# Kernel tuning notes

Measured on AMD Instinct MI355X. Metric: run time of the kernel, lower is better.

The kernel has to match this reference:

```python
import jax, jax.numpy as jnp
import numpy as np

N = 2048      # feature_num (nodes/sensors)
T = 5         # timd_num (window length)
D = 64        # embed_dim
TOPK = 21     # topk + 1 (includes self, cos(i,i)=1)
B = 32        # batch
EPS = 1e-5
NEG_SLOPE = 0.2


def setup_inputs() -> dict:
    key = jax.random.key(0)
    ks = jax.random.split(key, 9)
    s = 1.0 / np.sqrt(D)
    return {
        "x": jax.random.normal(ks[0], (B, N, T), jnp.float32),
        "emb": jax.random.normal(ks[1], (N, D), jnp.float32) * s,      # embedding table
        "W": jax.random.normal(ks[2], (D, T), jnp.float32) * (1.0 / np.sqrt(T)),  # GNN lin weight
        "Wb": jax.random.normal(ks[3], (D,), jnp.float32) * 0.01,       # GNN lin bias
        "a_src": jax.random.normal(ks[4], (2 * D,), jnp.float32) * s,   # attention vec (source half)
        "a_dst": jax.random.normal(ks[5], (2 * D,), jnp.float32) * s,   # attention vec (dest half)
        "gamma": jnp.ones((D,), jnp.float32),                            # BatchNorm1d weight
        "beta": jnp.zeros((D,), jnp.float32),                            # BatchNorm1d bias
        "fc_w": jax.random.normal(ks[6], (1, D), jnp.float32) * s,      # fc weight
        "fc_b": jnp.zeros((1,), jnp.float32),                            # fc bias
    }


def reference(x, emb, W, Wb, a_src, a_dst, gamma, beta, fc_w, fc_b):
    # --- cosine-sim topk graph build ---
    norm = jnp.linalg.norm(emb, axis=-1)                    # [N]
    cos = (emb @ emb.T) / (norm[:, None] * norm[None, :])   # [N,N]
    _, idx = jax.lax.top_k(cos, TOPK)                       # [N,TOPK]
    # scatter one-hot adjacency (vectorized, no per-row loop)
    adj = jnp.zeros((N, N), x.dtype).at[jnp.arange(N)[:, None], idx].set(1.0)
    # --- GNN: GDN-style attention message passing ---
    h = jnp.einsum('bnt,dt->bnd', x, W) + Wb                # [B,N,D]
    g = jnp.concatenate([h, jnp.broadcast_to(emb, h.shape)], axis=-1)  # [B,N,2D]
    e_src = g @ a_src                                       # [B,N]
    e_dst = g @ a_dst                                       # [B,N]
    e = jax.nn.leaky_relu(e_src[:, :, None] + e_dst[:, None, :], NEG_SLOPE)  # [B,N,N]
    e = jnp.where(adj > 0, e, jnp.float32(-1e9))
    alpha = jax.nn.softmax(e, axis=-1)                      # [B,N,N], rows sum to 1 over TOPK nbrs
    z = jax.nn.relu(jnp.einsum('bij,bjd->bid', alpha, h))   # [B,N,D]
    # --- output head: z * emb, BN over channels, relu, fc ---
    out = z * emb                                           # [B,N,D]
    mean = out.mean(axis=(0, 1))                            # BN1d stats over (batch, nodes)
    var = out.var(axis=(0, 1))
    out = (out - mean) * jax.lax.rsqrt(var + EPS) * gamma + beta
    out = jax.nn.relu(out)
    out = out @ fc_w.T + fc_b                               # [B,N,1]
    return out.reshape(-1, N)                               # [B,N]
```

## Files before the change

### kernel.cpp

```cpp
#include <hip/hip_runtime.h>
#include <math.h>

#define N_NODES 2048
#define T_WIN 5
#define D_EMB 64
#define TOPK 21
#define B_BATCH 32
#define BN_TOTAL (B_BATCH * N_NODES)
#define EPS_BN 1e-5f
#define NEG_SLOPE 0.2f
#define STATS_STRIDE 16

typedef unsigned long long u64;

__device__ __forceinline__ float wave_sum(float v) {
#pragma unroll
    for (int off = 32; off > 0; off >>= 1) v += __shfl_xor(v, off, 64);
    return v;
}

__device__ __forceinline__ u64 max64(u64 a, u64 b) { return a > b ? a : b; }
__device__ __forceinline__ u64 min64(u64 a, u64 b) { return a < b ? a : b; }

__device__ __forceinline__ u64 bitonic_sort64_desc(u64 key, int lane) {
#pragma unroll
    for (int k = 2; k <= 64; k <<= 1) {
#pragma unroll
        for (int j = k >> 1; j >= 1; j >>= 1) {
            u64 pk = __shfl_xor(key, j, 64);
            bool dirDesc = ((lane & k) == 0);
            bool keepMax = (((lane & j) == 0) == dirDesc);
            key = keepMax ? max64(key, pk) : min64(key, pk);
        }
    }
    return key;
}

__device__ __forceinline__ u64 bitonic_merge_top64(u64 a, u64 b, int lane) {
    u64 br = __shfl(b, 63 - lane, 64);
    u64 c = max64(a, br);
#pragma unroll
    for (int j = 32; j >= 1; j >>= 1) {
        u64 pk = __shfl_xor(c, j, 64);
        bool keepMax = ((lane & j) == 0);
        c = keepMax ? max64(c, pk) : min64(c, pk);
    }
    return c;
}

__global__ __launch_bounds__(256) void k_edge(
    const float* __restrict__ x, const float* __restrict__ W,
    const float* __restrict__ Wb, const float* __restrict__ a_src,
    const float* __restrict__ a_dst, const float* __restrict__ emb,
    float* __restrict__ es2T, float* __restrict__ ed2T,
    float* __restrict__ norms, float* __restrict__ stats,
    float* __restrict__ stats2) {
    if (blockIdx.x < 2) {
        float* p = blockIdx.x ? stats2 : stats;
        ((float4*)p)[threadIdx.x] = make_float4(0.f, 0.f, 0.f, 0.f);
    }
    int wid = threadIdx.x >> 6, lane = threadIdx.x & 63;
    int gw = blockIdx.x * 4 + wid;
    const float* wp = W + lane * T_WIN;
    float w0 = wp[0], w1 = wp[1], w2 = wp[2], w3 = wp[3], w4 = wp[4];
    float bias = Wb[lane];
    float as = a_src[lane], asE = a_src[D_EMB + lane];
    float ad = a_dst[lane], adE = a_dst[D_EMB + lane];

    for (int node = gw; node < BN_TOTAL; node += 8192) {
        int n = node & (N_NODES - 1);
        const float* xp = x + (size_t)node * T_WIN;
        float hv = bias + xp[0] * w0 + xp[1] * w1 + xp[2] * w2 + xp[3] * w3 + xp[4] * w4;
        float e = emb[n * D_EMB + lane];
        if (node < N_NODES) {
            float s2 = wave_sum(e * e);
            if (lane == 0) norms[node] = sqrtf(s2);
        }
        float es = wave_sum(hv * as + e * asE);
        float ed = wave_sum(hv * ad + e * adE);
        if (lane == 0) {
            es2T[node] = es;
            ed2T[node] = ed;
        }
    }
}

__global__ __launch_bounds__(256) void k_gram(
    const float* __restrict__ emb, const float* __restrict__ norms,
    float* __restrict__ cosM) {
    __shared__ __align__(16) float As[64][68];
    __shared__ __align__(16) float Bs[64][68];
    int t = threadIdx.x;
    int g = blockIdx.x;
    int a = (int)((sqrtf(8.f * g + 1.f) - 1.f) * 0.5f);
    while ((a + 1) * (a + 2) / 2 <= g) a++;
    while (a * (a + 1) / 2 > g) a--;
    int bq = g - a * (a + 1) / 2;
    int i0 = a * 64, j0 = bq * 64;

    {
        int r = t >> 2, c0 = t & 3;
        const float4* srcA = (const float4*)(emb + (size_t)(i0 + r) * D_EMB);
        const float4* srcB = (const float4*)(emb + (size_t)(j0 + r) * D_EMB);
#pragma unroll
        for (int k = 0; k < 4; k++) {
            int f4 = c0 + 4 * k;
            float4 v = srcA[f4];
            int d = 4 * f4;
            As[d][r] = v.x; As[d + 1][r] = v.y; As[d + 2][r] = v.z; As[d + 3][r] = v.w;
            float4 w = srcB[f4];
            Bs[d][r] = w.x; Bs[d + 1][r] = w.y; Bs[d + 2][r] = w.z; Bs[d + 3][r] = w.w;
        }
    }
    __syncthreads();

    int ti = t & 15, tj = t >> 4;
    float acc[4][4] = {};
#pragma unroll
    for (int d = 0; d < 64; d++) {
        float4 av = *(const float4*)&As[d][4 * ti];
        float4 bv = *(const float4*)&Bs[d][4 * tj];
        acc[0][0] += av.x * bv.x; acc[0][1] += av.x * bv.y; acc[0][2] += av.x * bv.z; acc[0][3] += av.x * bv.w;
        acc[1][0] += av.y * bv.x; acc[1][1] += av.y * bv.y; acc[1][2] += av.y * bv.z; acc[1][3] += av.y * bv.w;
        acc[2][0] += av.z * bv.x; acc[2][1] += av.z * bv.y; acc[2][2] += av.z * bv.z; acc[2][3] += av.z * bv.w;
        acc[3][0] += av.w * bv.x; acc[3][1] += av.w * bv.y; acc[3][2] += av.w * bv.z; acc[3][3] += av.w * bv.w;
    }

    float nis[4] = {norms[i0 + 4 * ti], norms[i0 + 4 * ti + 1],
                    norms[i0 + 4 * ti + 2], norms[i0 + 4 * ti + 3]};
    float njs[4] = {norms[j0 + 4 * tj], norms[j0 + 4 * tj + 1],
                    norms[j0 + 4 * tj + 2], norms[j0 + 4 * tj + 3]};
#pragma unroll
    for (int r = 0; r < 4; r++) {
        float4 o;
        o.x = acc[r][0] / (nis[r] * njs[0]);
        o.y = acc[r][1] / (nis[r] * njs[1]);
        o.z = acc[r][2] / (nis[r] * njs[2]);
        o.w = acc[r][3] / (nis[r] * njs[3]);
        int i = i0 + 4 * ti + r;
        *(float4*)(cosM + (size_t)i * N_NODES + j0 + 4 * tj) = o;
        cosM[(size_t)(j0 + 4 * tj + 0) * N_NODES + i] = o.x;
        cosM[(size_t)(j0 + 4 * tj + 1) * N_NODES + i] = o.y;
        cosM[(size_t)(j0 + 4 * tj + 2) * N_NODES + i] = o.z;
        cosM[(size_t)(j0 + 4 * tj + 3) * N_NODES + i] = o.w;
    }
}

__global__ __launch_bounds__(256) void k_select(
    const float* __restrict__ cosM, int* __restrict__ idxT) {
    __shared__ u64 candbuf[4][128];
    __shared__ u64 mbuf[2][64];
    int tid = threadIdx.x;
    int wid = tid >> 6, lane = tid & 63;
    int pair = wid >> 1;
    int half = wid & 1;
    int i = blockIdx.x * 2 + pair;
    int jbase = half * (N_NODES / 2);
    const float* row = cosM + (size_t)i * N_NODES + jbase;
    u64* buf = candbuf[wid];

    u64 a = 0;
    u64 t = 0;
    int cnt = 0;
    float vcur = row[lane];

#pragma unroll 1
    for (int c = 0; c < N_NODES / 128; c++) {
        int j = c * 64 + lane;
        float v = vcur;
        if (c < N_NODES / 128 - 1) vcur = row[j + 64];
        unsigned u = __float_as_uint(v);
        u = (u & 0x80000000u) ? ~u : (u | 0x80000000u);
        u64 key = ((u64)u << 32) | (unsigned)(~(j + jbase));
        unsigned long long ball = __ballot(key > t);
        if (ball) {
            int ofs = __popcll(ball & ((1ull << lane) - 1ull));
            if (key > t) buf[cnt + ofs] = key;
            cnt += (int)__popcll(ball);
            if (cnt >= 64) {
                u64 nk = buf[lane];
                nk = bitonic_sort64_desc(nk, lane);
                a = bitonic_merge_top64(a, nk, lane);
                t = __shfl(a, 20, 64);
                int rem = cnt - 64;
                u64 mv = (lane < rem) ? buf[64 + lane] : 0;
                if (lane < rem) buf[lane] = mv;
                cnt = rem;
            }
        }
    }
    while (cnt > 0) {
        int take = cnt < 64 ? cnt : 64;
        u64 nk = (lane < take) ? buf[lane] : 0;
        nk = bitonic_sort64_desc(nk, lane);
        a = bitonic_merge_top64(a, nk, lane);
        t = __shfl(a, 20, 64);
        int rem = cnt - take;
        u64 mv = (lane < rem) ? buf[take + lane] : 0;
        if (lane < rem) buf[lane] = mv;
        cnt = rem;
    }

    if (half) mbuf[pair][lane] = a;
    __syncthreads();
    if (!half) {
        u64 bv = mbuf[pair][lane];
        a = bitonic_merge_top64(a, bv, lane);
        if (lane < TOPK) idxT[lane * N_NODES + i] = (int)(~(unsigned)a);
    }
}

__global__ __launch_bounds__(256) void k_alpha(
    const int* __restrict__ idxT, const float* __restrict__ es2T,
    const float* __restrict__ ed2T, float* __restrict__ alphaT) {
    __shared__ float sed[N_NODES];
    int g = blockIdx.x;
    int b = g & 31;
    int i0 = (g >> 5) * 256;
    int t = threadIdx.x;

    {
        const float4* src = (const float4*)(ed2T + (size_t)b * N_NODES);
        float4* dst = (float4*)sed;
#pragma unroll
        for (int q = 0; q < 2; q++) dst[t + 256 * q] = src[t + 256 * q];
    }
    __syncthreads();

    int i = i0 + t;
    float es = es2T[(size_t)b * N_NODES + i];
    float ev[TOPK];
    float m = -3e38f;
#pragma unroll
    for (int k = 0; k < TOPK; k++) {
        int jk = idxT[k * N_NODES + i];
        float e = es + sed[jk];
        e = e > 0.f ? e : NEG_SLOPE * e;
        ev[k] = e;
        m = fmaxf(m, e);
    }
    float s = 0.f;
#pragma unroll
    for (int k = 0; k < TOPK; k++) {
        ev[k] = __expf(ev[k] - m);
        s += ev[k];
    }
    float inv = 1.0f / s;
#pragma unroll
    for (int k = 0; k < TOPK; k++)
        alphaT[((size_t)b * TOPK + k) * N_NODES + i] = ev[k] * inv;
}

__global__ __launch_bounds__(256, 2) void k_msg(
    const float* __restrict__ x, const float* __restrict__ W,
    const float* __restrict__ Wb, const int* __restrict__ idxT,
    const float* __restrict__ alphaT, const float* __restrict__ emb,
    float* __restrict__ obufT, float* __restrict__ stats,
    float* __restrict__ stats2) {
    __shared__ float hts[N_NODES][6];
    __shared__ float sred[2][4][4];

    int g = blockIdx.x;
    int b = (g & 7) + 8 * ((g >> 3) & 3);
    int c = g >> 5;
    int d0 = c * 4;
    int t = threadIdx.x;
    int wid = t >> 6, lane = t & 63;

    float wc[4][T_WIN], wb4[4];
#pragma unroll
    for (int q = 0; q < 4; q++) {
        wb4[q] = Wb[d0 + q];
#pragma unroll
        for (int tt = 0; tt < T_WIN; tt++) wc[q][tt] = W[(d0 + q) * T_WIN + tt];
    }
    const float* xb = x + (size_t)b * N_NODES * T_WIN;
#pragma unroll
    for (int r = 0; r < 8; r++) {
        int row = t + 256 * r;
        const float* xr = xb + row * T_WIN;
        float x0 = xr[0], x1 = xr[1], x2 = xr[2], x3 = xr[3], x4 = xr[4];
        float h0 = wb4[0] + x0 * wc[0][0] + x1 * wc[0][1] + x2 * wc[0][2] + x3 * wc[0][3] + x4 * wc[0][4];
        float h1 = wb4[1] + x0 * wc[1][0] + x1 * wc[1][1] + x2 * wc[1][2] + x3 * wc[1][3] + x4 * wc[1][4];
        float h2 = wb4[2] + x0 * wc[2][0] + x1 * wc[2][1] + x2 * wc[2][2] + x3 * wc[2][3] + x4 * wc[2][4];
        float h3 = wb4[3] + x0 * wc[3][0] + x1 * wc[3][1] + x2 * wc[3][2] + x3 * wc[3][3] + x4 * wc[3][4];
        *(float2*)&hts[row][0] = make_float2(h0, h1);
        *(float2*)&hts[row][2] = make_float2(h2, h3);
    }
    __syncthreads();

    float sacc[4] = {0.f, 0.f, 0.f, 0.f};
    float sacc2[4] = {0.f, 0.f, 0.f, 0.f};
    const float* aT = alphaT + (size_t)b * TOPK * N_NODES;
#pragma unroll 1
    for (int r = 0; r < 8; r++) {
        int i = 256 * r + t;
        float4 z = make_float4(0.f, 0.f, 0.f, 0.f);
#pragma unroll
        for (int k = 0; k < TOPK; k++) {
            int jk = idxT[k * N_NODES + i];
            float a = aT[(size_t)k * N_NODES + i];
            float2 h01 = *(const float2*)&hts[jk][0];
            float2 h23 = *(const float2*)&hts[jk][2];
            z.x = fmaf(a, h01.x, z.x);
            z.y = fmaf(a, h01.y, z.y);
            z.z = fmaf(a, h23.x, z.z);
            z.w = fmaf(a, h23.y, z.w);
        }
        float4 e4 = *(const float4*)(emb + (size_t)i * D_EMB + d0);
        float4 o;
        o.x = fmaxf(z.x, 0.f) * e4.x;
        o.y = fmaxf(z.y, 0.f) * e4.y;
        o.z = fmaxf(z.z, 0.f) * e4.z;
        o.w = fmaxf(z.w, 0.f) * e4.w;
        ((float4*)obufT)[((size_t)c * B_BATCH + b) * N_NODES + i] = o;
        sacc[0] += o.x; sacc[1] += o.y; sacc[2] += o.z; sacc[3] += o.w;
        sacc2[0] += o.x * o.x; sacc2[1] += o.y * o.y;
        sacc2[2] += o.z * o.z; sacc2[3] += o.w * o.w;
    }

#pragma unroll
    for (int q = 0; q < 4; q++) {
        sacc[q] = wave_sum(sacc[q]);
        sacc2[q] = wave_sum(sacc2[q]);
    }
    if (lane == 0) {
#pragma unroll
        for (int q = 0; q < 4; q++) {
            sred[0][wid][q] = sacc[q];
            sred[1][wid][q] = sacc2[q];
        }
    }
    __syncthreads();
    if (t < 8) {
        int q = t & 3, which = t >> 2;
        float v = sred[which][0][q] + sred[which][1][q] + sred[which][2][q] + sred[which][3][q];
        float* dst = which ? stats2 : stats;
        atomicAdd(&dst[(d0 + q) * STATS_STRIDE], v);
    }
}

__global__ __launch_bounds__(256) void k_out(
    const float* __restrict__ obufT, const float* __restrict__ stats,
    const float* __restrict__ stats2, const float* __restrict__ gamma,
    const float* __restrict__ beta, const float* __restrict__ fc_w,
    const float* __restrict__ fc_b, float* __restrict__ out) {
    __shared__ float smean[64], sinv[64], sg[64], sb[64], sf[64];
    int t = threadIdx.x;
    int g = blockIdx.x;
    int b = g & 31, nc = g >> 5;
    int n = nc * 256 + t;
    const float invM = 1.0f / (float)BN_TOTAL;

    if (t < 64) {
        float mn = stats[t * STATS_STRIDE] * invM;
        float var = stats2[t * STATS_STRIDE] * invM - mn * mn;
        smean[t] = mn;
        sinv[t] = rsqrtf(var + EPS_BN);
        sg[t] = gamma[t]; sb[t] = beta[t]; sf[t] = fc_w[t];
    }
    __syncthreads();

    float fb = fc_b[0];
    float p = 0.f;
#pragma unroll
    for (int c = 0; c < 16; c++) {
        float4 o = ((const float4*)obufT)[((size_t)c * B_BATCH + b) * N_NODES + n];
        int d = 4 * c;
        float v;
        v = fmaxf((o.x - smean[d + 0]) * sinv[d + 0] * sg[d + 0] + sb[d + 0], 0.f); p = fmaf(v, sf[d + 0], p);
        v = fmaxf((o.y - smean[d + 1]) * sinv[d + 1] * sg[d + 1] + sb[d + 1], 0.f); p = fmaf(v, sf[d + 1], p);
        v = fmaxf((o.z - smean[d + 2]) * sinv[d + 2] * sg[d + 2] + sb[d + 2], 0.f); p = fmaf(v, sf[d + 2], p);
        v = fmaxf((o.w - smean[d + 3]) * sinv[d + 3] * sg[d + 3] + sb[d + 3], 0.f); p = fmaf(v, sf[d + 3], p);
    }
    out[b * N_NODES + n] = p + fb;
}

extern "C" void kernel_launch(void* const* d_in, const int* in_sizes, int n_in,
                              void* d_out, int out_size, void* d_ws, size_t ws_size,
                              hipStream_t stream) {
    const float* x     = (const float*)d_in[0];
    const float* emb   = (const float*)d_in[1];
    const float* W     = (const float*)d_in[2];
    const float* Wb    = (const float*)d_in[3];
    const float* a_src = (const float*)d_in[4];
    const float* a_dst = (const float*)d_in[5];
    const float* gamma = (const float*)d_in[6];
    const float* beta  = (const float*)d_in[7];
    const float* fc_w  = (const float*)d_in[8];
    const float* fc_b  = (const float*)d_in[9];
    float* out = (float*)d_out;

    char* ws = (char*)d_ws;
    float* stats  = (float*)(ws + 0);
    float* stats2 = (float*)(ws + 4096);
    int*   idxT   = (int*)  (ws + 8192);
    float* norms  = (float*)(ws + 180224);
    float* es2T   = (float*)(ws + 188416);
    float* ed2T   = (float*)(ws + 450560);
    float* alphaT = (float*)(ws + 712704);
    float* cosM   = (float*)(ws + 6217728);
    float* obufT  = cosM;

    k_edge<<<2048, 256, 0, stream>>>(x, W, Wb, a_src, a_dst, emb,
                                     es2T, ed2T, norms, stats, stats2);
    k_gram<<<528, 256, 0, stream>>>(emb, norms, cosM);
    k_select<<<N_NODES / 2, 256, 0, stream>>>(cosM, idxT);
    k_alpha<<<256, 256, 0, stream>>>(idxT, es2T, ed2T, alphaT);
    k_msg<<<512, 256, 0, stream>>>(x, W, Wb, idxT, alphaT, emb, obufT, stats, stats2);
    k_out<<<256, 256, 0, stream>>>(obufT, stats, stats2, gamma, beta, fc_w, fc_b, out);
}
```

Before: 145.6 us.

## Fold attention vectors into W to precompute per-timestep edge score weights

```diff
diff --git a/kernel.cpp b/kernel.cpp
--- a/kernel.cpp
+++ b/kernel.cpp
@@ -48,40 +48,61 @@
     return c;
 }
 
-__global__ __launch_bounds__(256) void k_edge(
+__global__ __launch_bounds__(256) void k_pre(
     const float* __restrict__ x, const float* __restrict__ W,
     const float* __restrict__ Wb, const float* __restrict__ a_src,
     const float* __restrict__ a_dst, const float* __restrict__ emb,
-    float* __restrict__ es2T, float* __restrict__ ed2T,
+    float* __restrict__ xs2T, float* __restrict__ xd2T,
+    float* __restrict__ es_embP, float* __restrict__ ed_embP,
     float* __restrict__ norms, float* __restrict__ stats,
     float* __restrict__ stats2) {
-    if (blockIdx.x < 2) {
-        float* p = blockIdx.x ? stats2 : stats;
-        ((float4*)p)[threadIdx.x] = make_float4(0.f, 0.f, 0.f, 0.f);
-    }
-    int wid = threadIdx.x >> 6, lane = threadIdx.x & 63;
-    int gw = blockIdx.x * 4 + wid;
-    const float* wp = W + lane * T_WIN;
-    float w0 = wp[0], w1 = wp[1], w2 = wp[2], w3 = wp[3], w4 = wp[4];
-    float bias = Wb[lane];
-    float as = a_src[lane], asE = a_src[D_EMB + lane];
-    float ad = a_dst[lane], adE = a_dst[D_EMB + lane];
-
-    for (int node = gw; node < BN_TOTAL; node += 8192) {
-        int n = node & (N_NODES - 1);
-        const float* xp = x + (size_t)node * T_WIN;
-        float hv = bias + xp[0] * w0 + xp[1] * w1 + xp[2] * w2 + xp[3] * w3 + xp[4] * w4;
-        float e = emb[n * D_EMB + lane];
-        if (node < N_NODES) {
-            float s2 = wave_sum(e * e);
-            if (lane == 0) norms[node] = sqrtf(s2);
-        }
-        float es = wave_sum(hv * as + e * asE);
-        float ed = wave_sum(hv * ad + e * adE);
+    int t = threadIdx.x;
+    if (blockIdx.x < 512) {
+        if (blockIdx.x < 2) {
+            float* p = blockIdx.x ? stats2 : stats;
+            ((float4*)p)[t] = make_float4(0.f, 0.f, 0.f, 0.f);
+        }
+        int wid = t >> 6, lane = t & 63;
+        int node = blockIdx.x * 4 + wid;
+        float e = emb[node * D_EMB + lane];
+        float s2 = wave_sum(e * e);
+        float esE = wave_sum(e * a_src[D_EMB + lane]);
+        float edE = wave_sum(e * a_dst[D_EMB + lane]);
         if (lane == 0) {
-            es2T[node] = es;
-            ed2T[node] = ed;
-        }
+            norms[node] = sqrtf(s2);
+            es_embP[node] = esE;
+            ed_embP[node] = edE;
+        }
+        return;
+    }
+
+    __shared__ float cws[5], cwd[5], cbs[2];
+    if (t < 12) {
+        int which = (t < 5 || t == 10) ? 0 : 1;
+        const float* av = which ? a_dst : a_src;
+        const float* sp;
+        int stride;
+        if (t < 10) { int tt = (t < 5) ? t : t - 5; sp = W + tt; stride = T_WIN; }
+        else        { sp = Wb; stride = 1; }
+        float acc = 0.f;
+        for (int d = 0; d < D_EMB; d++) acc += sp[d * stride] * av[d];
+        if (t < 5)       cws[t] = acc;
+        else if (t < 10) cwd[t - 5] = acc;
+        else             cbs[t - 10] = acc;
+    }
+    __syncthreads();
+    float ws0 = cws[0], ws1 = cws[1], ws2 = cws[2], ws3 = cws[3], ws4 = cws[4];
+    float wd0 = cwd[0], wd1 = cwd[1], wd2 = cwd[2], wd3 = cwd[3], wd4 = cwd[4];
+    float bss = cbs[0], bsd = cbs[1];
+
+    int base = (blockIdx.x - 512) * 1024;
+#pragma unroll
+    for (int r = 0; r < 4; r++) {
+        int item = base + 256 * r + t;
+        const float* xp = x + (size_t)item * T_WIN;
+        float x0 = xp[0], x1 = xp[1], x2 = xp[2], x3 = xp[3], x4 = xp[4];
+        xs2T[item] = bss + x0 * ws0 + x1 * ws1 + x2 * ws2 + x3 * ws3 + x4 * ws4;
+        xd2T[item] = bsd + x0 * wd0 + x1 * wd1 + x2 * wd2 + x3 * wd3 + x4 * wd4;
     }
 }
 
@@ -211,8 +232,9 @@
 }
 
 __global__ __launch_bounds__(256) void k_alpha(
-    const int* __restrict__ idxT, const float* __restrict__ es2T,
-    const float* __restrict__ ed2T, float* __restrict__ alphaT) {
+    const int* __restrict__ idxT, const float* __restrict__ xs2T,
+    const float* __restrict__ xd2T, const float* __restrict__ es_embP,
+    const float* __restrict__ ed_embP, float* __restrict__ alphaT) {
     __shared__ float sed[N_NODES];
     int g = blockIdx.x;
     int b = g & 31;
@@ -220,15 +242,21 @@
     int t = threadIdx.x;
 
     {
-        const float4* src = (const float4*)(ed2T + (size_t)b * N_NODES);
+        const float4* sxd = (const float4*)(xd2T + (size_t)b * N_NODES);
+        const float4* sde = (const float4*)(ed_embP);
         float4* dst = (float4*)sed;
 #pragma unroll
-        for (int q = 0; q < 2; q++) dst[t + 256 * q] = src[t + 256 * q];
+        for (int q = 0; q < 2; q++) {
+            int idx = t + 256 * q;
+            float4 u = sxd[idx];
+            float4 v = sde[idx];
+            dst[idx] = make_float4(u.x + v.x, u.y + v.y, u.z + v.z, u.w + v.w);
+        }
     }
     __syncthreads();
 
     int i = i0 + t;
-    float es = es2T[(size_t)b * N_NODES + i];
+    float es = xs2T[(size_t)b * N_NODES + i] + es_embP[i];
     float ev[TOPK];
     float m = -3e38f;
 #pragma unroll
@@ -392,21 +420,24 @@
     float* out = (float*)d_out;
 
     char* ws = (char*)d_ws;
-    float* stats  = (float*)(ws + 0);
-    float* stats2 = (float*)(ws + 4096);
-    int*   idxT   = (int*)  (ws + 8192);
-    float* norms  = (float*)(ws + 180224);
-    float* es2T   = (float*)(ws + 188416);
-    float* ed2T   = (float*)(ws + 450560);
-    float* alphaT = (float*)(ws + 712704);
-    float* cosM   = (float*)(ws + 6217728);
-    float* obufT  = cosM;
-
-    k_edge<<<2048, 256, 0, stream>>>(x, W, Wb, a_src, a_dst, emb,
-                                     es2T, ed2T, norms, stats, stats2);
+    float* stats   = (float*)(ws + 0);
+    float* stats2  = (float*)(ws + 4096);
+    int*   idxT    = (int*)  (ws + 8192);
+    float* norms   = (float*)(ws + 180224);
+    float* es_embP = (float*)(ws + 188416);
+    float* ed_embP = (float*)(ws + 196608);
+    float* xs2T    = (float*)(ws + 204800);
+    float* xd2T    = (float*)(ws + 466944);
+    float* alphaT  = (float*)(ws + 729088);
+    float* cosM    = (float*)(ws + 6234112);
+    float* obufT   = cosM;
+
+    k_pre<<<576, 256, 0, stream>>>(x, W, Wb, a_src, a_dst, emb,
+                                   xs2T, xd2T, es_embP, ed_embP, norms,
+                                   stats, stats2);
     k_gram<<<528, 256, 0, stream>>>(emb, norms, cosM);
     k_select<<<N_NODES / 2, 256, 0, stream>>>(cosM, idxT);
-    k_alpha<<<256, 256, 0, stream>>>(idxT, es2T, ed2T, alphaT);
+    k_alpha<<<256, 256, 0, stream>>>(idxT, xs2T, xd2T, es_embP, ed_embP, alphaT);
     k_msg<<<512, 256, 0, stream>>>(x, W, Wb, idxT, alphaT, emb, obufT, stats, stats2);
     k_out<<<256, 256, 0, stream>>>(obufT, stats, stats2, gamma, beta, fc_w, fc_b, out);
 }
```

New measurement: 137.1 us. 5.9% less time.
